# Kernel tuning notes

Hardware: AMD Instinct MI355X
Metric: run time of the kernel (lower is better)

Reference implementation:

```python
import jax, jax.numpy as jnp
import numpy as np

RADIUS = 2.5          # radial_score radius from the call site
CORRECT_THRESHOLD = 0.5  # DetectionF1Metric.correct_threshold (assumed; sigmoid(radius-d)=0.5 at d=radius)


def setup_inputs() -> dict:
    key = jax.random.key(0)
    k1, k2, k3, k4, k5 = jax.random.split(key, 5)
    B, P, T = 16, 4096, 1024
    # pred rows: [class, x, y, conf_logit]
    pred_cls = jax.random.randint(k1, (B, P), 0, 2).astype(jnp.float32)
    pred_xy = jax.random.uniform(k2, (B, P, 2), dtype=jnp.float32) * 512.0
    conf = jax.random.normal(k3, (B, P), dtype=jnp.float32)
    pred = jnp.concatenate([pred_cls[..., None], pred_xy, conf[..., None]], axis=-1)
    # gt rows: [class, x, y]
    gt_cls = jax.random.randint(k4, (B, T), 0, 2).astype(jnp.float32)
    gt_xy = jax.random.uniform(k5, (B, T, 2), dtype=jnp.float32) * 512.0
    gt = jnp.concatenate([gt_cls[..., None], gt_xy], axis=-1)
    return {"pred": pred, "gt": gt}


def _bce_with_logits(logits, targets):
    # mean of max(x,0) - x*y + log(1+exp(-|x|)), numerically stable
    return jnp.mean(jnp.maximum(logits, 0.0) - logits * targets
                    + jnp.log1p(jnp.exp(-jnp.abs(logits))))


def _per_image(pred_b, gt_b):
    classes = pred_b[:, 0]          # [P]
    centers = pred_b[:, 1:3]        # [P,2]
    confs = pred_b[:, 3]            # [P]
    tcls = gt_b[:, 0]               # [T]
    txy = gt_b[:, 1:3]              # [T,2]
    P = classes.shape[0]
    # pairwise radial score (sigmoid form): scores[p,t] in [P,T]
    d = jnp.sqrt(jnp.sum((centers[:, None, :] - txy[None, :, :]) ** 2, axis=-1) + 1e-12)
    scores = jax.nn.sigmoid(RADIUS - d)
    valid = (scores >= CORRECT_THRESHOLD) & (classes[:, None] == tcls[None, :])
    masked = jnp.where(valid, scores, -jnp.inf)
    # greedy dedup: best-scoring pred per target (equivalent to sort-desc + unique per
    # the torch code only drops duplicate rows, which doesn't change `correct`).
    best_pred_per_t = jnp.argmax(masked, axis=0)          # [T]
    any_valid_t = jnp.any(valid, axis=0)                  # [T]
    hits = jnp.zeros((P,), jnp.int32).at[best_pred_per_t].add(any_valid_t.astype(jnp.int32))
    correct = hits > 0                                    # [P] bool
    # reg target uses the UNMASKED per-pred max score, only where correct
    reg = jnp.where(correct, jnp.max(scores, axis=1), 0.0)
    obj_loss = _bce_with_logits(confs, correct.astype(jnp.float32))
    reg_loss = jnp.mean(1.0 - reg)
    return obj_loss, reg_loss


def reference(pred, gt):
    obj_b, reg_b = jax.vmap(_per_image)(pred, gt)
    obj_loss = jnp.mean(obj_b)
    reg_loss = jnp.mean(reg_b)
    return obj_loss, reg_loss
```

## Files before the change

### kernel.cpp

```cpp
#include <hip/hip_runtime.h>
#include <math.h>


#define NB 16
#define NP 4096
#define NT 1024
#define MAGIC 0x5CA1AB1Eu

#define O_WFLAGS 0
#define O_PART   (NB * NP * 4)

__global__ __launch_bounds__(1024) void k_all(
    const float4* __restrict__ pred, const float* __restrict__ gt,
    unsigned* __restrict__ wflags, float* __restrict__ partials)
{
    const int bid = blockIdx.x;
    const int b = bid >> 2, q = bid & 3;
    const int tid = threadIdx.x, lane = tid & 63, wave = tid >> 6;

    __shared__ unsigned short scnt[4096];
    __shared__ unsigned short sbins[4096];
    __shared__ float2 sxy[NT];
    __shared__ unsigned short slist[256];
    __shared__ unsigned scount;
    __shared__ unsigned wsum[16];
    __shared__ float pc[2];

    const float4* pb = pred + (size_t)b * NP;
    const float*  gb = gt + (size_t)b * NT * 3;

    ((unsigned*)scnt)[tid] = 0u;
    ((unsigned*)scnt)[tid + 1024] = 0u;
    if (tid == 0) scount = 0u;
    if (tid < 2) pc[tid] = 0.0f;
    sxy[tid] = make_float2(gb[3 * tid + 1], gb[3 * tid + 2]);
    __syncthreads();

    int cellc[4];
    float lb = 0.0f;
    #pragma unroll
    for (int k = 0; k < 4; k++) {
        float4 pr = pb[tid + 1024 * k];
        int cell = (int)(pr.y * 0.125f) + ((int)(pr.z * 0.125f) << 6);
        cellc[k] = cell;
        atomicAdd((unsigned*)scnt + (cell >> 1), (cell & 1) ? 0x10000u : 1u);
        if (k == q) {
            float x = pr.w;
            lb = fmaxf(x, 0.0f) + log1pf(expf(-fabsf(x)));
        }
    }
    for (int off = 32; off; off >>= 1) lb += __shfl_down(lb, off, 64);
    if (lane == 0) atomicAdd(&pc[0], lb);
    __syncthreads();

    {
        int base = tid * 4;
        unsigned loc[4], s = 0;
        #pragma unroll
        for (int i = 0; i < 4; i++) { loc[i] = s; s += (unsigned)scnt[base + i]; }
        unsigned v = s;
        for (int off = 1; off < 64; off <<= 1) {
            unsigned o = __shfl_up(v, off, 64);
            if (lane >= off) v += o;
        }
        if (lane == 63) wsum[wave] = v;
        __syncthreads();
        unsigned wbase = 0;
        for (int w = 0; w < wave; w++) wbase += wsum[w];
        unsigned tbase = wbase + v - s;
        #pragma unroll
        for (int i = 0; i < 4; i++) scnt[base + i] = (unsigned short)(tbase + loc[i]);
    }
    __syncthreads();

    #pragma unroll
    for (int k = 0; k < 4; k++) {
        int cell = cellc[k];
        unsigned old = atomicAdd((unsigned*)scnt + (cell >> 1), (cell & 1) ? 0x10000u : 1u);
        sbins[(cell & 1) ? (old >> 16) : (old & 0xFFFFu)] = (unsigned short)(tid + 1024 * k);
    }
    __syncthreads();

    if (tid < 256) {
        const int t = q * 256 + tid;
        float tcl = gb[3 * t];
        float2 txy = sxy[t];
        float tx = txy.x, ty = txy.y;
        int x0 = (int)floorf((tx - 2.51f) * 0.125f); if (x0 < 0) x0 = 0;
        int x1 = (int)((tx + 2.51f) * 0.125f);       if (x1 > 63) x1 = 63;
        int y0 = (int)floorf((ty - 2.51f) * 0.125f); if (y0 < 0) y0 = 0;
        int y1 = (int)((ty + 2.51f) * 0.125f);       if (y1 > 63) y1 = 63;
        float bd = 3.0e38f; int bp = 0x7fffffff;
        for (int cy = y0; cy <= y1; cy++)
            for (int cx = x0; cx <= x1; cx++) {
                int c = cx + (cy << 6);
                unsigned s0 = c ? (unsigned)scnt[c - 1] : 0u;
                unsigned s1 = (unsigned)scnt[c];
                for (unsigned k = s0; k < s1; k++) {
                    int p = sbins[k];
                    float4 pr = pb[p];
                    if (pr.x == tcl) {
                        float dx = pr.y - tx, dy = pr.z - ty;
                        float d2 = fmaf(dy, dy, dx * dx);
                        if (d2 < bd || (d2 == bd && p < bp)) { bd = d2; bp = p; }
                    }
                }
            }
        if (bd <= 6.25f) {
            unsigned old = atomicExch(&wflags[b * NP + bp], MAGIC);
            if (old != MAGIC)
                slist[atomicAdd(&scount, 1u)] = (unsigned short)bp;
        }
    }
    __syncthreads();

    {
        unsigned n = scount;
        float lc = 0.0f, ls = 0.0f;
        for (unsigned e = (unsigned)wave; e < n; e += 16) {
            int p = slist[e];
            float4 pr = pb[p];
            float md = 1.0e30f;
            #pragma unroll 4
            for (int t = lane; t < NT; t += 64) {
                float2 xy = sxy[t];
                float dx = pr.y - xy.x, dy = pr.z - xy.y;
                md = fminf(md, fmaf(dy, dy, dx * dx));
            }
            for (int off = 32; off; off >>= 1)
                md = fminf(md, __shfl_down(md, off, 64));
            if (lane == 0) {
                float dd = sqrtf(md + 1e-12f);
                ls += 1.0f / (1.0f + expf(dd - 2.5f));
                lc += pr.w;
            }
        }
        if (lane == 0 && (lc != 0.0f || ls != 0.0f)) {
            atomicAdd(&pc[0], -lc);
            atomicAdd(&pc[1], ls);
        }
    }
    __syncthreads();

    if (tid == 0) {
        partials[bid]      = pc[0];
        partials[64 + bid] = pc[1];
    }
}

__global__ __launch_bounds__(128) void k_fin(const float* __restrict__ partials,
                                             float* __restrict__ out) {
    const int lane = threadIdx.x & 63, wave = threadIdx.x >> 6;
    float v = partials[wave * 64 + lane];
    for (int off = 32; off; off >>= 1) v += __shfl_down(v, off, 64);
    if (lane == 0) {
        const float inv = 1.0f / (float)(NB * NP);
        if (wave == 0) out[0] = v * inv;
        else           out[1] = 1.0f - v * inv;
    }
}

extern "C" void kernel_launch(void* const* d_in, const int* in_sizes, int n_in,
                              void* d_out, int out_size, void* d_ws, size_t ws_size,
                              hipStream_t stream) {
    const float4* pred = (const float4*)d_in[0];
    const float*  gt   = (const float*)d_in[1];
    char* w = (char*)d_ws;
    unsigned* wflags  = (unsigned*)(w + O_WFLAGS);
    float*    partials = (float*)(w + O_PART);

    k_all<<<4 * NB, 1024, 0, stream>>>(pred, gt, wflags, partials);
    k_fin<<<1, 128, 0, stream>>>(partials, (float*)d_out);
}
```

Baseline: 74.04 us.

## Cache class-signed pred coords in LDS, split cell search, fuse final reduction

Binned prediction coordinates are now copied into shared memory, with the class encoded in the sign bit of x, and ground truth is staged with coalesced loads. The neighbour search no longer gathers predictions from global memory. The search is spread across all 1024 threads, four lanes per target, each scanning one grid cell, with a shuffle reduction to pick the best prediction. The separate finalize kernel is replaced by a last-block reduction that uses done flags and a guard flag in the workspace. This removes a launch and the global gathers, but relies on the workspace flags being zeroed on every call.

Result: faster. 69.34 us (-6.3%).

```diff
diff --git a/kernel.cpp b/kernel.cpp
--- a/kernel.cpp
+++ b/kernel.cpp
@@ -9,10 +9,14 @@
 
 #define O_WFLAGS 0
 #define O_PART   (NB * NP * 4)
+#define O_DONE   (O_PART + 128 * 4)
+#define O_FGUARD (O_DONE + 64 * 4)
 
 __global__ __launch_bounds__(1024) void k_all(
     const float4* __restrict__ pred, const float* __restrict__ gt,
-    unsigned* __restrict__ wflags, float* __restrict__ partials)
+    unsigned* __restrict__ wflags, float* __restrict__ partials,
+    unsigned* __restrict__ done, unsigned* __restrict__ fguard,
+    float* __restrict__ out)
 {
     const int bid = blockIdx.x;
     const int b = bid >> 2, q = bid & 3;
@@ -20,6 +24,7 @@
 
     __shared__ unsigned short scnt[4096];
     __shared__ unsigned short sbins[4096];
+    __shared__ float2 spxy[4096];
     __shared__ float2 sxy[NT];
     __shared__ unsigned short slist[256];
     __shared__ unsigned scount;
@@ -28,19 +33,29 @@
 
     const float4* pb = pred + (size_t)b * NP;
     const float*  gb = gt + (size_t)b * NT * 3;
+    float* sraw = (float*)spxy;
 
     ((unsigned*)scnt)[tid] = 0u;
     ((unsigned*)scnt)[tid + 1024] = 0u;
     if (tid == 0) scount = 0u;
     if (tid < 2) pc[tid] = 0.0f;
-    sxy[tid] = make_float2(gb[3 * tid + 1], gb[3 * tid + 2]);
-    __syncthreads();
-
+    sraw[tid]        = gb[tid];
+    sraw[tid + 1024] = gb[tid + 1024];
+    sraw[tid + 2048] = gb[tid + 2048];
+    __syncthreads();
+
+    {
+        float c = sraw[3 * tid], x = sraw[3 * tid + 1], y = sraw[3 * tid + 2];
+        sxy[tid] = make_float2(c != 0.0f ? -x : x, y);
+    }
+
+    float4 prv[4];
     int cellc[4];
     float lb = 0.0f;
     #pragma unroll
     for (int k = 0; k < 4; k++) {
         float4 pr = pb[tid + 1024 * k];
+        prv[k] = pr;
         int cell = (int)(pr.y * 0.125f) + ((int)(pr.z * 0.125f) << 6);
         cellc[k] = cell;
         atomicAdd((unsigned*)scnt + (cell >> 1), (cell & 1) ? 0x10000u : 1u);
@@ -77,36 +92,46 @@
     for (int k = 0; k < 4; k++) {
         int cell = cellc[k];
         unsigned old = atomicAdd((unsigned*)scnt + (cell >> 1), (cell & 1) ? 0x10000u : 1u);
-        sbins[(cell & 1) ? (old >> 16) : (old & 0xFFFFu)] = (unsigned short)(tid + 1024 * k);
-    }
-    __syncthreads();
-
-    if (tid < 256) {
-        const int t = q * 256 + tid;
-        float tcl = gb[3 * t];
+        unsigned slot = (cell & 1) ? (old >> 16) : (old & 0xFFFFu);
+        sbins[slot] = (unsigned short)(tid + 1024 * k);
+        float4 pr = prv[k];
+        spxy[slot] = make_float2(pr.x != 0.0f ? -pr.y : pr.y, pr.z);
+    }
+    __syncthreads();
+
+    {
+        const int t = q * 256 + (tid >> 2);
+        const int j = tid & 3;
         float2 txy = sxy[t];
-        float tx = txy.x, ty = txy.y;
+        const int tsign = __float_as_int(txy.x);
+        const float tx = fabsf(txy.x), ty = txy.y;
         int x0 = (int)floorf((tx - 2.51f) * 0.125f); if (x0 < 0) x0 = 0;
         int x1 = (int)((tx + 2.51f) * 0.125f);       if (x1 > 63) x1 = 63;
         int y0 = (int)floorf((ty - 2.51f) * 0.125f); if (y0 < 0) y0 = 0;
         int y1 = (int)((ty + 2.51f) * 0.125f);       if (y1 > 63) y1 = 63;
         float bd = 3.0e38f; int bp = 0x7fffffff;
-        for (int cy = y0; cy <= y1; cy++)
-            for (int cx = x0; cx <= x1; cx++) {
-                int c = cx + (cy << 6);
-                unsigned s0 = c ? (unsigned)scnt[c - 1] : 0u;
-                unsigned s1 = (unsigned)scnt[c];
-                for (unsigned k = s0; k < s1; k++) {
+        const int cx = x0 + (j & 1), cy = y0 + (j >> 1);
+        if (cx <= x1 && cy <= y1) {
+            const int c = cx + (cy << 6);
+            unsigned s0 = c ? (unsigned)scnt[c - 1] : 0u;
+            unsigned s1 = (unsigned)scnt[c];
+            for (unsigned k = s0; k < s1; k++) {
+                float2 pxy = spxy[k];
+                if (((__float_as_int(pxy.x) ^ tsign) & 0x80000000) == 0) {
+                    float dx = fabsf(pxy.x) - tx, dy = pxy.y - ty;
+                    float d2 = fmaf(dy, dy, dx * dx);
                     int p = sbins[k];
-                    float4 pr = pb[p];
-                    if (pr.x == tcl) {
-                        float dx = pr.y - tx, dy = pr.z - ty;
-                        float d2 = fmaf(dy, dy, dx * dx);
-                        if (d2 < bd || (d2 == bd && p < bp)) { bd = d2; bp = p; }
-                    }
+                    if (d2 < bd || (d2 == bd && p < bp)) { bd = d2; bp = p; }
                 }
             }
-        if (bd <= 6.25f) {
+        }
+        #pragma unroll
+        for (int m = 1; m <= 2; m <<= 1) {
+            float od = __shfl_xor(bd, m, 64);
+            int   op = __shfl_xor(bp, m, 64);
+            if (od < bd || (od == bd && op < bp)) { bd = od; bp = op; }
+        }
+        if (j == 0 && bd <= 6.25f) {
             unsigned old = atomicExch(&wflags[b * NP + bp], MAGIC);
             if (old != MAGIC)
                 slist[atomicAdd(&scount, 1u)] = (unsigned short)bp;
@@ -124,7 +149,7 @@
             #pragma unroll 4
             for (int t = lane; t < NT; t += 64) {
                 float2 xy = sxy[t];
-                float dx = pr.y - xy.x, dy = pr.z - xy.y;
+                float dx = pr.y - fabsf(xy.x), dy = pr.z - xy.y;
                 md = fminf(md, fmaf(dy, dy, dx * dx));
             }
             for (int off = 32; off; off >>= 1)
@@ -143,20 +168,30 @@
     __syncthreads();
 
     if (tid == 0) {
-        partials[bid]      = pc[0];
-        partials[64 + bid] = pc[1];
-    }
-}
-
-__global__ __launch_bounds__(128) void k_fin(const float* __restrict__ partials,
-                                             float* __restrict__ out) {
-    const int lane = threadIdx.x & 63, wave = threadIdx.x >> 6;
-    float v = partials[wave * 64 + lane];
-    for (int off = 32; off; off >>= 1) v += __shfl_down(v, off, 64);
-    if (lane == 0) {
-        const float inv = 1.0f / (float)(NB * NP);
-        if (wave == 0) out[0] = v * inv;
-        else           out[1] = 1.0f - v * inv;
+        atomicExch(&partials[bid], pc[0]);
+        atomicExch(&partials[64 + bid], pc[1]);
+        __threadfence();
+        atomicExch(&done[bid], MAGIC);
+    }
+    if (wave == 0) {
+        asm volatile("s_waitcnt vmcnt(0)" ::: "memory");
+        unsigned f = (lane == bid) ? MAGIC : atomicAdd(&done[lane], 0u);
+        if (__ballot(f == MAGIC) == ~0ull) {
+            int win = 0;
+            if (lane == 0) win = (atomicExch(fguard, MAGIC) != MAGIC) ? 1 : 0;
+            if (__shfl(win, 0, 64)) {
+                __threadfence();
+                float v0 = atomicAdd(&partials[lane], 0.0f);
+                for (int off = 32; off; off >>= 1) v0 += __shfl_down(v0, off, 64);
+                float v1 = atomicAdd(&partials[64 + lane], 0.0f);
+                for (int off = 32; off; off >>= 1) v1 += __shfl_down(v1, off, 64);
+                if (lane == 0) {
+                    const float inv = 1.0f / (float)(NB * NP);
+                    out[0] = v0 * inv;
+                    out[1] = 1.0f - v1 * inv;
+                }
+            }
+        }
     }
 }
 
@@ -166,9 +201,10 @@
     const float4* pred = (const float4*)d_in[0];
     const float*  gt   = (const float*)d_in[1];
     char* w = (char*)d_ws;
-    unsigned* wflags  = (unsigned*)(w + O_WFLAGS);
+    unsigned* wflags   = (unsigned*)(w + O_WFLAGS);
     float*    partials = (float*)(w + O_PART);
-
-    k_all<<<4 * NB, 1024, 0, stream>>>(pred, gt, wflags, partials);
-    k_fin<<<1, 128, 0, stream>>>(partials, (float*)d_out);
+    unsigned* done     = (unsigned*)(w + O_DONE);
+    unsigned* fguard   = (unsigned*)(w + O_FGUARD);
+
+    k_all<<<4 * NB, 1024, 0, stream>>>(pred, gt, wflags, partials, done, fguard, (float*)d_out);
 }
```
